# Performance work log

Hardware: AMD Instinct MI355X
Metric: run time of the kernel (lower is better)

## Reference

```python
import jax, jax.numpy as jnp
import numpy as np

B = 4096      # batch
NS = 40       # number of single-valued features (length=1)
NM = 8        # number of multi-valued features
L = 8         # length of each multi-valued feature
V = 10000     # vocab per feature (table rows = V+1, row 0 = padding)
D = 64        # per-feature embedding dim (get_emb_dim(10000,64) == 64)
T = 16        # num_ns_tokens
DM = 512      # d_model
TOTAL = (NS + NM) * D      # 3072, total_emb_dim (pad = 0)
CHUNK = TOTAL // T         # 192, chunk_dim
LN_EPS = 1e-5


def setup_inputs() -> dict:
    key = jax.random.key(0)
    ks = jax.random.split(key, 10)
    int_feats = jax.random.randint(ks[0], (B, NS + NM * L), 0, V + 1)
    emb_single = jax.random.normal(ks[1], (NS, V + 1, D), jnp.float32) * 0.02
    emb_multi = jax.random.normal(ks[2], (NM, V + 1, D), jnp.float32) * 0.02
    h = TOTAL // 4
    lhuc_w1 = jax.random.normal(ks[3], (TOTAL, h), jnp.float32) * 0.02
    lhuc_b1 = jnp.zeros((h,), jnp.float32)
    lhuc_w2 = jax.random.normal(ks[4], (h, TOTAL), jnp.float32) * 0.02
    lhuc_b2 = jnp.zeros((TOTAL,), jnp.float32)
    proj_w = jax.random.normal(ks[5], (T, CHUNK, DM), jnp.float32) * 0.05
    proj_b = jnp.zeros((T, DM), jnp.float32)
    ln_g = jnp.ones((T, DM), jnp.float32)
    ln_b = jnp.zeros((T, DM), jnp.float32)
    return {
        "int_feats": int_feats,
        "emb_single": emb_single, "emb_multi": emb_multi,
        "lhuc_w1": lhuc_w1, "lhuc_b1": lhuc_b1,
        "lhuc_w2": lhuc_w2, "lhuc_b2": lhuc_b2,
        "proj_w": proj_w, "proj_b": proj_b, "ln_g": ln_g, "ln_b": ln_b,
    }


def reference(int_feats, emb_single, emb_multi, lhuc_w1, lhuc_b1,
              lhuc_w2, lhuc_b2, proj_w, proj_b, ln_g, ln_b):
    b = int_feats.shape[0]
    # --- single-valued features: per-feature gather (padding_idx=0 -> zero) ---
    idx_s = int_feats[:, :NS]                                   # (B, NS)
    es = emb_single[jnp.arange(NS)[None, :], idx_s]             # (B, NS, D)
    es = es * (idx_s != 0)[..., None].astype(es.dtype)
    # --- multi-valued features: gather + masked mean pool ---
    idx_m = int_feats[:, NS:].reshape(b, NM, L)                 # (B, NM, L)
    em = emb_multi[jnp.arange(NM)[None, :, None], idx_m]        # (B, NM, L, D)
    mask = (idx_m != 0)[..., None].astype(em.dtype)             # (B, NM, L, 1)
    denom = jnp.maximum(mask.sum(axis=2), 1.0)                  # (B, NM, 1)
    pooled = (em * mask).sum(axis=2) / denom                    # (B, NM, D)
    # --- concat (group order == feature order) ---
    cat = jnp.concatenate([es.reshape(b, NS * D), pooled.reshape(b, NM * D)], axis=-1)  # (B, TOTAL)
    # --- LHUC gating MLP ---
    h = jax.nn.silu(cat @ lhuc_w1 + lhuc_b1)
    gate = jax.nn.sigmoid(h @ lhuc_w2 + lhuc_b2)
    x = (cat * gate * 2.0).reshape(b, T, CHUNK)                 # pad == 0
    # --- per-token Linear + LayerNorm (batched over tokens) ---
    y = jnp.einsum('btc,tcd->btd', x, proj_w) + proj_b          # (B, T, DM)
    mu = y.mean(axis=-1, keepdims=True)
    var = ((y - mu) ** 2).mean(axis=-1, keepdims=True)
    y = (y - mu) * jax.lax.rsqrt(var + LN_EPS) * ln_g + ln_b
    return y
```

## Files before the change

### kernel.cpp

```cpp
#include <hip/hip_runtime.h>
#include <hip/hip_bf16.h>


typedef unsigned short u16;
typedef unsigned int u32;
typedef __attribute__((ext_vector_type(8))) short s16x8;
typedef __attribute__((ext_vector_type(4))) float f32x4;

#define NSF 40
#define NMF 8
#define LLEN 8
#define VROWS 10001
#define DD 64
#define TT 16
#define DMOD 512
#define TOTAL 3072
#define CHUNKC 192
#define NFEAT 104

__device__ __forceinline__ u16 f2bf(float f) {
  __hip_bfloat16 h = __float2bfloat16(f);
  return *reinterpret_cast<u16*>(&h);
}
__device__ __forceinline__ float bf2f(u16 u) {
  __hip_bfloat16 h;
  *reinterpret_cast<u16*>(&h) = u;
  return __bfloat162float(h);
}

__device__ __forceinline__ void gll16(const u16* g, u16* l) {
  __builtin_amdgcn_global_load_lds((const __attribute__((address_space(1))) void*)g,
                                   (__attribute__((address_space(3))) void*)l, 16, 0, 0);
}

__global__ void transpose_cast_kernel(const float* __restrict__ src, u16* __restrict__ dst,
                                      int R, int C, long srcStride, long dstStride) {
  __shared__ float tile[32][33];
  const float* s = src + (long)blockIdx.z * srcStride;
  u16* d = dst + (long)blockIdx.z * dstStride;
  int c0 = blockIdx.x * 32, r0 = blockIdx.y * 32;
#pragma unroll
  for (int i = 0; i < 32; i += 8)
    tile[threadIdx.y + i][threadIdx.x] = s[(long)(r0 + threadIdx.y + i) * C + c0 + threadIdx.x];
  __syncthreads();
#pragma unroll
  for (int i = 0; i < 32; i += 8)
    d[(long)(c0 + threadIdx.y + i) * R + r0 + threadIdx.x] = f2bf(tile[threadIdx.x][threadIdx.y + i]);
}

__global__ __launch_bounds__(256) void embed_kernel(const int* __restrict__ feats,
                                                    const float* __restrict__ tabS,
                                                    const float* __restrict__ tabM,
                                                    u16* __restrict__ catb) {
  int b = blockIdx.x;
  int tid = threadIdx.x;
  int d2 = tid & 31;
  int g = tid >> 5;
  const int* fr = feats + (long)b * NFEAT;
  u16* crow = catb + (long)b * TOTAL;

  for (int f = g; f < NSF; f += 8) {
    int idx = fr[f];
    float x = 0.f, y = 0.f;
    if (idx) {
      const float* e = tabS + ((long)f * VROWS + idx) * DD + d2 * 2;
      x = e[0]; y = e[1];
    }
    u32 pk = (u32)f2bf(x) | ((u32)f2bf(y) << 16);
    *reinterpret_cast<u32*>(crow + f * DD + d2 * 2) = pk;
  }
  int m = g;
  float sx = 0.f, sy = 0.f;
  int cnt = 0;
#pragma unroll
  for (int l = 0; l < LLEN; l++) {
    int idx = fr[NSF + m * LLEN + l];
    if (idx) {
      const float* e = tabM + ((long)m * VROWS + idx) * DD + d2 * 2;
      sx += e[0]; sy += e[1]; cnt++;
    }
  }
  float inv = 1.f / fmaxf((float)cnt, 1.f);
  u32 pk = (u32)f2bf(sx * inv) | ((u32)f2bf(sy * inv) << 16);
  *reinterpret_cast<u32*>(crow + NSF * DD + m * DD + d2 * 2) = pk;
}

template <int N, int K, int BM, int BN, int EPI>
__global__ __launch_bounds__(256) void gemm_kernel(const u16* __restrict__ A,
                                                   const u16* __restrict__ Bt,
                                                   const float* __restrict__ bias,
                                                   const u16* __restrict__ aux,
                                                   u16* __restrict__ Out) {
  constexpr int WCOL = (BN >= 128) ? 2 : 1;
  constexpr int WROW = 4 / WCOL;
  constexpr int MF = (BM / WROW) / 16;
  constexpr int NF = (BN / WCOL) / 16;
  constexpr int NT = K / 32;

  __shared__ u16 lA[2][BM * 32];
  __shared__ u16 lB[2][BN * 32];

  const int tid = threadIdx.x;
  const int w = tid >> 6;
  const int lane = tid & 63;
  const int l15 = lane & 15, hi = lane >> 4;
  const int wr = w / WCOL, wc = w % WCOL;
  const int m0 = blockIdx.y * BM, n0 = blockIdx.x * BN;

  f32x4 acc[MF][NF];
#pragma unroll
  for (int m = 0; m < MF; m++)
#pragma unroll
    for (int n = 0; n < NF; n++) acc[m][n] = (f32x4){0.f, 0.f, 0.f, 0.f};

  const int srow = tid >> 2;
  const int sc8 = (tid & 3) * 8;

  auto stage = [&](int buf, int t) {
    const u16* Ab = A + (long)m0 * K + t * 32;
    const u16* Bb = Bt + (long)n0 * K + t * 32;
#pragma unroll
    for (int i = 0; i < BM / 64; i++)
      gll16(Ab + (long)(i * 64 + srow) * K + sc8, &lA[buf][(i * 256 + w * 64) * 8]);
#pragma unroll
    for (int i = 0; i < BN / 64; i++)
      gll16(Bb + (long)(i * 64 + srow) * K + sc8, &lB[buf][(i * 256 + w * 64) * 8]);
  };

  stage(0, 0);
  __syncthreads();

#pragma unroll 2
  for (int t = 0; t < NT; t++) {
    int buf = t & 1;
    if (t + 1 < NT) stage(buf ^ 1, t + 1);
    s16x8 af[MF], bf[NF];
#pragma unroll
    for (int m = 0; m < MF; m++)
      af[m] = *reinterpret_cast<const s16x8*>(&lA[buf][(wr * (MF * 16) + m * 16 + l15) * 32 + hi * 8]);
#pragma unroll
    for (int n = 0; n < NF; n++)
      bf[n] = *reinterpret_cast<const s16x8*>(&lB[buf][(wc * (NF * 16) + n * 16 + l15) * 32 + hi * 8]);
#pragma unroll
    for (int m = 0; m < MF; m++)
#pragma unroll
      for (int n = 0; n < NF; n++)
        acc[m][n] = __builtin_amdgcn_mfma_f32_16x16x32_bf16(af[m], bf[n], acc[m][n], 0, 0, 0);
    __syncthreads();
  }

#pragma unroll
  for (int n = 0; n < NF; n++) {
    int col = n0 + wc * (NF * 16) + n * 16 + l15;
    float bs = bias[col];
#pragma unroll
    for (int m = 0; m < MF; m++) {
      int rbase = m0 + wr * (MF * 16) + m * 16 + hi * 4;
#pragma unroll
      for (int j = 0; j < 4; j++) {
        int row = rbase + j;
        float z = acc[m][n][j] + bs;
        float o;
        if (EPI == 0) {
          o = z / (1.f + __expf(-z));
        } else {
          float gs = 1.f / (1.f + __expf(-z));
          float xv = bf2f(aux[(long)row * N + col]);
          o = xv * gs * 2.f;
        }
        Out[(long)row * N + col] = f2bf(o);
      }
    }
  }
}

__global__ __launch_bounds__(512) void proj_ln_kernel(const u16* __restrict__ xb,
                                                      const u16* __restrict__ pwt,
                                                      const float* __restrict__ pb,
                                                      const float* __restrict__ lng,
                                                      const float* __restrict__ lnb,
                                                      float* __restrict__ out) {
  __shared__ u16 lA[2][64 * 32];
  __shared__ u16 lB[2][512 * 32];
  __shared__ float sred[64][4][2];

  const int t = blockIdx.y;
  const int m0 = blockIdx.x * 64;
  const int tid = threadIdx.x;
  const int w = tid >> 6, lane = tid & 63;
  const int l15 = lane & 15, hi = lane >> 4;
  const int wr = w >> 2, wc = w & 3;

  const u16* Ab = xb + (long)m0 * TOTAL + t * CHUNKC;
  const u16* Bb = pwt + (long)t * DMOD * CHUNKC;

  const int srow = tid >> 2;
  const int sc8 = (tid & 3) * 8;

  auto stage = [&](int buf, int kt) {
    if (w < 4)
      gll16(Ab + (long)srow * TOTAL + kt * 32 + sc8, &lA[buf][w * 512]);
#pragma unroll
    for (int i = 0; i < 4; i++)
      gll16(Bb + (long)(i * 128 + srow) * CHUNKC + kt * 32 + sc8,
            &lB[buf][i * 4096 + w * 512]);
  };

  f32x4 acc[2][8];
#pragma unroll
  for (int m = 0; m < 2; m++)
#pragma unroll
    for (int n = 0; n < 8; n++) acc[m][n] = (f32x4){0.f, 0.f, 0.f, 0.f};

  stage(0, 0);
  __syncthreads();

#pragma unroll
  for (int kt = 0; kt < 6; kt++) {
    int buf = kt & 1;
    if (kt + 1 < 6) stage(buf ^ 1, kt + 1);
    s16x8 af[2], bfr[8];
#pragma unroll
    for (int m = 0; m < 2; m++)
      af[m] = *reinterpret_cast<const s16x8*>(&lA[buf][(wr * 32 + m * 16 + l15) * 32 + hi * 8]);
#pragma unroll
    for (int n = 0; n < 8; n++)
      bfr[n] = *reinterpret_cast<const s16x8*>(&lB[buf][(wc * 128 + n * 16 + l15) * 32 + hi * 8]);
#pragma unroll
    for (int m = 0; m < 2; m++)
#pragma unroll
      for (int n = 0; n < 8; n++)
        acc[m][n] = __builtin_amdgcn_mfma_f32_16x16x32_bf16(af[m], bfr[n], acc[m][n], 0, 0, 0);
    __syncthreads();
  }

  float sum[2][4], sq[2][4];
#pragma unroll
  for (int m = 0; m < 2; m++)
#pragma unroll
    for (int j = 0; j < 4; j++) { sum[m][j] = 0.f; sq[m][j] = 0.f; }

#pragma unroll
  for (int n = 0; n < 8; n++) {
    float bs = pb[t * DMOD + wc * 128 + n * 16 + l15];
#pragma unroll
    for (int m = 0; m < 2; m++)
#pragma unroll
      for (int j = 0; j < 4; j++) {
        float v = acc[m][n][j] + bs;
        acc[m][n][j] = v;
        sum[m][j] += v;
        sq[m][j] += v * v;
      }
  }
#pragma unroll
  for (int m = 0; m < 2; m++)
#pragma unroll
    for (int j = 0; j < 4; j++) {
#pragma unroll
      for (int o = 1; o < 16; o <<= 1) {
        sum[m][j] += __shfl_xor(sum[m][j], o, 64);
        sq[m][j] += __shfl_xor(sq[m][j], o, 64);
      }
    }
  if (l15 == 0) {
#pragma unroll
    for (int m = 0; m < 2; m++)
#pragma unroll
      for (int j = 0; j < 4; j++) {
        int r = wr * 32 + m * 16 + hi * 4 + j;
        sred[r][wc][0] = sum[m][j];
        sred[r][wc][1] = sq[m][j];
      }
  }
  __syncthreads();

  float mean[2][4], rstd[2][4];
#pragma unroll
  for (int m = 0; m < 2; m++)
#pragma unroll
    for (int j = 0; j < 4; j++) {
      int r = wr * 32 + m * 16 + hi * 4 + j;
      float s = sred[r][0][0] + sred[r][1][0] + sred[r][2][0] + sred[r][3][0];
      float q = sred[r][0][1] + sred[r][1][1] + sred[r][2][1] + sred[r][3][1];
      float mu = s * (1.f / 512.f);
      float var = q * (1.f / 512.f) - mu * mu;
      mean[m][j] = mu;
      rstd[m][j] = rsqrtf(var + 1e-5f);
    }
#pragma unroll
  for (int n = 0; n < 8; n++) {
    int c = wc * 128 + n * 16 + l15;
    float g = lng[t * DMOD + c], bb = lnb[t * DMOD + c];
#pragma unroll
    for (int m = 0; m < 2; m++)
#pragma unroll
      for (int j = 0; j < 4; j++) {
        int r = wr * 32 + m * 16 + hi * 4 + j;
        float o = (acc[m][n][j] - mean[m][j]) * rstd[m][j] * g + bb;
        out[((long)(m0 + r) * TT + t) * DMOD + c] = o;
      }
  }
}

extern "C" void kernel_launch(void* const* d_in, const int* in_sizes, int n_in,
                              void* d_out, int out_size, void* d_ws, size_t ws_size,
                              hipStream_t stream) {
  const int* feats = (const int*)d_in[0];
  const float* embS = (const float*)d_in[1];
  const float* embM = (const float*)d_in[2];
  const float* w1 = (const float*)d_in[3];
  const float* b1 = (const float*)d_in[4];
  const float* w2 = (const float*)d_in[5];
  const float* b2 = (const float*)d_in[6];
  const float* pw = (const float*)d_in[7];
  const float* pb = (const float*)d_in[8];
  const float* lng = (const float*)d_in[9];
  const float* lnb = (const float*)d_in[10];
  float* out = (float*)d_out;

  char* p = (char*)d_ws;
  u16* catb = (u16*)p; p += (size_t)4096 * 3072 * 2;
  u16* hb   = (u16*)p; p += (size_t)4096 * 768 * 2;
  u16* xb   = (u16*)p; p += (size_t)4096 * 3072 * 2;
  u16* w1t  = (u16*)p; p += (size_t)768 * 3072 * 2;
  u16* w2t  = (u16*)p; p += (size_t)3072 * 768 * 2;
  u16* pwt  = (u16*)p; p += (size_t)16 * 512 * 192 * 2;

  transpose_cast_kernel<<<dim3(768 / 32, 3072 / 32, 1), dim3(32, 8), 0, stream>>>(
      w1, w1t, 3072, 768, 0, 0);
  transpose_cast_kernel<<<dim3(3072 / 32, 768 / 32, 1), dim3(32, 8), 0, stream>>>(
      w2, w2t, 768, 3072, 0, 0);
  transpose_cast_kernel<<<dim3(512 / 32, 192 / 32, 16), dim3(32, 8), 0, stream>>>(
      pw, pwt, 192, 512, 192 * 512, 192 * 512);

  embed_kernel<<<4096, 256, 0, stream>>>(feats, embS, embM, catb);

  gemm_kernel<768, 3072, 64, 64, 0><<<dim3(768 / 64, 4096 / 64), 256, 0, stream>>>(
      catb, w1t, b1, nullptr, hb);

  gemm_kernel<3072, 768, 128, 128, 1><<<dim3(3072 / 128, 4096 / 128), 256, 0, stream>>>(
      hb, w2t, b2, catb, xb);

  proj_ln_kernel<<<dim3(4096 / 64, 16), 512, 0, stream>>>(xb, pwt, pb, lng, lnb, out);
}
```

Before: 421.5 us.

## Merge weight transposes, vectorize embedding gather, swizzle block order, enlarge GEMM1 tiles

The three transpose-cast launches are merged into one kernel that dispatches on block index, saving two launches. The embedding gather now loads float4 per thread, and the multi-valued pooling is split across two half-groups joined by a shuffle. GEMM and proj/LN blocks are remapped in an XCD-style interleave so neighbouring tiles land on the same die. The first GEMM moves from 64x64 to 128x128 tiles, which may cut its block count to 192 and leave some of the device idle.

```diff
diff --git a/kernel.cpp b/kernel.cpp
--- a/kernel.cpp
+++ b/kernel.cpp
@@ -33,19 +33,25 @@
                                    (__attribute__((address_space(3))) void*)l, 16, 0, 0);
 }
 
-__global__ void transpose_cast_kernel(const float* __restrict__ src, u16* __restrict__ dst,
-                                      int R, int C, long srcStride, long dstStride) {
+__global__ void transpose_all_kernel(const float* __restrict__ w1, u16* __restrict__ w1t,
+                                     const float* __restrict__ w2, u16* __restrict__ w2t,
+                                     const float* __restrict__ pw, u16* __restrict__ pwt) {
   __shared__ float tile[32][33];
-  const float* s = src + (long)blockIdx.z * srcStride;
-  u16* d = dst + (long)blockIdx.z * dstStride;
-  int c0 = blockIdx.x * 32, r0 = blockIdx.y * 32;
+  int id = blockIdx.x;
+  const float* src; u16* dst; int R, C, bx, by;
+  if (id < 2304)      { src = w1; dst = w1t; R = 3072; C = 768;  bx = id % 24; by = id / 24; }
+  else if (id < 4608) { int l = id - 2304; src = w2; dst = w2t; R = 768; C = 3072; bx = l % 96; by = l / 96; }
+  else                { int l = id - 4608; int t = l / 96; int r2 = l % 96;
+                        src = pw + (long)t * CHUNKC * DMOD; dst = pwt + (long)t * DMOD * CHUNKC;
+                        R = CHUNKC; C = DMOD; bx = r2 % 16; by = r2 / 16; }
+  int c0 = bx * 32, r0 = by * 32;
 #pragma unroll
   for (int i = 0; i < 32; i += 8)
-    tile[threadIdx.y + i][threadIdx.x] = s[(long)(r0 + threadIdx.y + i) * C + c0 + threadIdx.x];
+    tile[threadIdx.y + i][threadIdx.x] = src[(long)(r0 + threadIdx.y + i) * C + c0 + threadIdx.x];
   __syncthreads();
 #pragma unroll
   for (int i = 0; i < 32; i += 8)
-    d[(long)(c0 + threadIdx.y + i) * R + r0 + threadIdx.x] = f2bf(tile[threadIdx.x][threadIdx.y + i]);
+    dst[(long)(c0 + threadIdx.y + i) * R + r0 + threadIdx.x] = f2bf(tile[threadIdx.x][threadIdx.y + i]);
 }
 
 __global__ __launch_bounds__(256) void embed_kernel(const int* __restrict__ feats,
@@ -54,35 +60,38 @@
                                                     u16* __restrict__ catb) {
   int b = blockIdx.x;
   int tid = threadIdx.x;
-  int d2 = tid & 31;
-  int g = tid >> 5;
+  int d4 = tid & 15;
+  int g = tid >> 4;
   const int* fr = feats + (long)b * NFEAT;
   u16* crow = catb + (long)b * TOTAL;
 
-  for (int f = g; f < NSF; f += 8) {
+  for (int f = g; f < NSF; f += 16) {
     int idx = fr[f];
-    float x = 0.f, y = 0.f;
+    float4 v = make_float4(0.f, 0.f, 0.f, 0.f);
+    if (idx) v = *reinterpret_cast<const float4*>(tabS + ((long)f * VROWS + idx) * DD + d4 * 4);
+    ushort4 pk = {f2bf(v.x), f2bf(v.y), f2bf(v.z), f2bf(v.w)};
+    *reinterpret_cast<ushort4*>(crow + f * DD + d4 * 4) = pk;
+  }
+  int m = g >> 1, half = g & 1;
+  float sx = 0.f, sy = 0.f, sz = 0.f, sw = 0.f, cnt = 0.f;
+#pragma unroll
+  for (int l = 0; l < 4; l++) {
+    int idx = fr[NSF + m * LLEN + half * 4 + l];
     if (idx) {
-      const float* e = tabS + ((long)f * VROWS + idx) * DD + d2 * 2;
-      x = e[0]; y = e[1];
+      float4 e = *reinterpret_cast<const float4*>(tabM + ((long)m * VROWS + idx) * DD + d4 * 4);
+      sx += e.x; sy += e.y; sz += e.z; sw += e.w; cnt += 1.f;
     }
-    u32 pk = (u32)f2bf(x) | ((u32)f2bf(y) << 16);
-    *reinterpret_cast<u32*>(crow + f * DD + d2 * 2) = pk;
-  }
-  int m = g;
-  float sx = 0.f, sy = 0.f;
-  int cnt = 0;
-#pragma unroll
-  for (int l = 0; l < LLEN; l++) {
-    int idx = fr[NSF + m * LLEN + l];
-    if (idx) {
-      const float* e = tabM + ((long)m * VROWS + idx) * DD + d2 * 2;
-      sx += e[0]; sy += e[1]; cnt++;
-    }
-  }
-  float inv = 1.f / fmaxf((float)cnt, 1.f);
-  u32 pk = (u32)f2bf(sx * inv) | ((u32)f2bf(sy * inv) << 16);
-  *reinterpret_cast<u32*>(crow + NSF * DD + m * DD + d2 * 2) = pk;
+  }
+  sx += __shfl_xor(sx, 16, 64);
+  sy += __shfl_xor(sy, 16, 64);
+  sz += __shfl_xor(sz, 16, 64);
+  sw += __shfl_xor(sw, 16, 64);
+  cnt += __shfl_xor(cnt, 16, 64);
+  if (!half) {
+    float inv = 1.f / fmaxf(cnt, 1.f);
+    ushort4 pk = {f2bf(sx * inv), f2bf(sy * inv), f2bf(sz * inv), f2bf(sw * inv)};
+    *reinterpret_cast<ushort4*>(crow + NSF * DD + m * DD + d4 * 4) = pk;
+  }
 }
 
 template <int N, int K, int BM, int BN, int EPI>
@@ -105,7 +114,11 @@
   const int lane = tid & 63;
   const int l15 = lane & 15, hi = lane >> 4;
   const int wr = w / WCOL, wc = w % WCOL;
-  const int m0 = blockIdx.y * BM, n0 = blockIdx.x * BN;
+
+  const int nblk = gridDim.x * gridDim.y;
+  const int lid = blockIdx.x + gridDim.x * blockIdx.y;
+  const int sw = (lid & 7) * (nblk >> 3) + (lid >> 3);
+  const int m0 = (sw / gridDim.x) * BM, n0 = (sw % gridDim.x) * BN;
 
   f32x4 acc[MF][NF];
 #pragma unroll
@@ -184,12 +197,15 @@
   __shared__ u16 lB[2][512 * 32];
   __shared__ float sred[64][4][2];
 
-  const int t = blockIdx.y;
-  const int m0 = blockIdx.x * 64;
   const int tid = threadIdx.x;
   const int w = tid >> 6, lane = tid & 63;
   const int l15 = lane & 15, hi = lane >> 4;
   const int wr = w >> 2, wc = w & 3;
+
+  const int lid = blockIdx.x + gridDim.x * blockIdx.y;
+  const int sw = (lid & 7) * ((gridDim.x * gridDim.y) >> 3) + (lid >> 3);
+  const int t = sw / gridDim.x;
+  const int m0 = (sw % gridDim.x) * 64;
 
   const u16* Ab = xb + (long)m0 * TOTAL + t * CHUNKC;
   const u16* Bb = pwt + (long)t * DMOD * CHUNKC;
@@ -327,16 +343,11 @@
   u16* w2t  = (u16*)p; p += (size_t)3072 * 768 * 2;
   u16* pwt  = (u16*)p; p += (size_t)16 * 512 * 192 * 2;
 
-  transpose_cast_kernel<<<dim3(768 / 32, 3072 / 32, 1), dim3(32, 8), 0, stream>>>(
-      w1, w1t, 3072, 768, 0, 0);
-  transpose_cast_kernel<<<dim3(3072 / 32, 768 / 32, 1), dim3(32, 8), 0, stream>>>(
-      w2, w2t, 768, 3072, 0, 0);
-  transpose_cast_kernel<<<dim3(512 / 32, 192 / 32, 16), dim3(32, 8), 0, stream>>>(
-      pw, pwt, 192, 512, 192 * 512, 192 * 512);
+  transpose_all_kernel<<<6144, dim3(32, 8), 0, stream>>>(w1, w1t, w2, w2t, pw, pwt);
 
   embed_kernel<<<4096, 256, 0, stream>>>(feats, embS, embM, catb);
 
-  gemm_kernel<768, 3072, 64, 64, 0><<<dim3(768 / 64, 4096 / 64), 256, 0, stream>>>(
+  gemm_kernel<768, 3072, 128, 128, 0><<<dim3(768 / 128, 4096 / 128), 256, 0, stream>>>(
       catb, w1t, b1, nullptr, hb);
 
   gemm_kernel<3072, 768, 128, 128, 1><<<dim3(3072 / 128, 4096 / 128), 256, 0, stream>>>(
```

Measured after the change: 433.0 us. +2.7%, slower.
